# Performance work log

Measured on AMD Instinct MI355X. Metric: run time of the kernel, lower is better.

Reference implementation:

```python
import jax, jax.numpy as jnp
import numpy as np

N_NODES = 10000

def _gcn_norm(edges, n_nodes):
    # PyG GCNConv default: add self-loops, symmetric normalization D^-1/2 A_hat D^-1/2
    src, dst = edges[0], edges[1]
    loop = jnp.arange(n_nodes, dtype=src.dtype)
    src = jnp.concatenate([src, loop])
    dst = jnp.concatenate([dst, loop])
    deg = jax.ops.segment_sum(jnp.ones_like(dst, dtype=jnp.float32), dst, num_segments=n_nodes)
    dinv = jnp.where(deg > 0, jax.lax.rsqrt(deg), 0.0)
    norm = dinv[src] * dinv[dst]  # [E + N]
    return src, dst, norm

def _gcn_layer(x, src, dst, norm, W, b):
    # linear transform, then gather -> weight -> scatter-add aggregation
    x = x @ W  # [N, F]
    msg = x[src] * norm[:, None]  # [E+N, F]
    out = jax.ops.segment_sum(msg, dst, num_segments=x.shape[0])
    return out + b

def setup_inputs() -> dict:
    key = jax.random.key(0)
    k1, k2, k3, k4 = jax.random.split(key, 4)
    d = 128
    E = 640000
    scale = 1.0 / np.sqrt(d)
    return {
        "nodes_embeddings": jax.random.normal(k1, (N_NODES, d), dtype=jnp.float32),
        "edges": jax.random.randint(k2, (2, E), 0, N_NODES, dtype=jnp.int64),
        "W1": jax.random.normal(k3, (d, d), dtype=jnp.float32) * scale,
        "b1": jnp.zeros((d,), dtype=jnp.float32),
        "W2": jax.random.normal(k4, (d, d), dtype=jnp.float32) * scale,
        "b2": jnp.zeros((d,), dtype=jnp.float32),
    }

def reference(nodes_embeddings, edges, W1, b1, W2, b2):
    src, dst, norm = _gcn_norm(edges, nodes_embeddings.shape[0])
    x = _gcn_layer(nodes_embeddings, src, dst, norm, W1, b1)
    x = _gcn_layer(x, src, dst, norm, W2, b2)
    return x
```

## Files before the change

### kernel.cpp

```cpp
#include <hip/hip_runtime.h>
#include <hip/hip_bf16.h>

#define D 128
#define NBINS 157
#define BIN_CAP 5120
#define EPB 4096

__device__ __forceinline__ unsigned rne_bf16(float f) {
    unsigned u = __float_as_uint(f);
    return (u + 0x7FFFu + ((u >> 16) & 1u)) >> 16;
}
__device__ __forceinline__ float bf16_lo(unsigned u) { return __uint_as_float(u << 16); }
__device__ __forceinline__ float bf16_hi(unsigned u) { return __uint_as_float(u & 0xFFFF0000u); }

__global__ __launch_bounds__(512) void fused_gemm_scatter(
        const float* __restrict__ X, const float* __restrict__ W,
        float* __restrict__ Y,
        const int* __restrict__ src, const int* __restrict__ dst,
        int* __restrict__ binTotal, int* __restrict__ binned,
        int E, int N, int gGemm) {
    __shared__ float smem[D * D];
    int tid = threadIdx.x;

    if ((int)blockIdx.x < gGemm) {
        {
            const float4* W4 = (const float4*)W;
            float4* Ws4 = (float4*)smem;
            #pragma unroll
            for (int i = 0; i < 8; ++i)
                Ws4[tid + 512 * i] = W4[tid + 512 * i];
        }
        __syncthreads();
        const float2* Ws2 = (const float2*)smem;
        int col2 = tid & 63;
        int wv   = __builtin_amdgcn_readfirstlane(tid >> 6);
        int row0 = blockIdx.x * 32 + wv * 4;
        if (row0 >= N) return;

        const float4* xr[4];
        #pragma unroll
        for (int r = 0; r < 4; ++r) {
            int rr = row0 + r; if (rr > N - 1) rr = N - 1;
            xr[r] = (const float4*)(X + (size_t)rr * D);
        }
        float accx[4] = {0.f, 0.f, 0.f, 0.f};
        float accy[4] = {0.f, 0.f, 0.f, 0.f};
        #pragma unroll 8
        for (int kb = 0; kb < 32; ++kb) {
            float4 xv[4];
            #pragma unroll
            for (int r = 0; r < 4; ++r) xv[r] = xr[r][kb];
            #pragma unroll
            for (int kk = 0; kk < 4; ++kk) {
                float2 w = Ws2[(4 * kb + kk) * 64 + col2];
                #pragma unroll
                for (int r = 0; r < 4; ++r) {
                    float xs = ((const float*)&xv[r])[kk];
                    accx[r] = fmaf(xs, w.x, accx[r]);
                    accy[r] = fmaf(xs, w.y, accy[r]);
                }
            }
        }
        #pragma unroll
        for (int r = 0; r < 4; ++r) {
            int rr = row0 + r;
            if (rr < N)
                ((float2*)Y)[(size_t)rr * 64 + col2] = make_float2(accx[r], accy[r]);
        }
    } else {
        int* cnt   = (int*)smem;
        int* loff  = cnt + 160;
        int* gbase = cnt + 320;
        int* scur  = cnt + 480;
        int* stage = cnt + 640;
        for (int b = tid; b < NBINS; b += 512) cnt[b] = 0;
        __syncthreads();

        int bid = blockIdx.x - gGemm;
        int base = bid * EPB + tid * 8;
        int s[8], dl[8], bn[8];
        int ne = 0;
        if (base + 8 <= E) {
            const int4* s4 = (const int4*)(src + base);
            const int4* d4 = (const int4*)(dst + base);
            int4 a0 = s4[0], a1 = s4[1], c0 = d4[0], c1 = d4[1];
            int ss[8] = {a0.x, a0.y, a0.z, a0.w, a1.x, a1.y, a1.z, a1.w};
            int dd[8] = {c0.x, c0.y, c0.z, c0.w, c1.x, c1.y, c1.z, c1.w};
            ne = 8;
            #pragma unroll
            for (int i = 0; i < 8; ++i) { s[i] = ss[i]; bn[i] = dd[i] >> 6; dl[i] = dd[i] & 63; }
        } else {
            for (int i = 0; i < 8; ++i) {
                int e = base + i;
                if (e < E) { s[ne] = src[e]; int d = dst[e]; bn[ne] = d >> 6; dl[ne] = d & 63; ++ne; }
            }
        }
        for (int i = 0; i < ne; ++i) atomicAdd(&cnt[bn[i]], 1);
        __syncthreads();

        if (tid < NBINS) gbase[tid] = atomicAdd(&binTotal[tid], cnt[tid]);
        if (tid < 64) {
            int c0 = (3 * tid     < NBINS) ? cnt[3 * tid    ] : 0;
            int c1 = (3 * tid + 1 < NBINS) ? cnt[3 * tid + 1] : 0;
            int c2 = (3 * tid + 2 < NBINS) ? cnt[3 * tid + 2] : 0;
            int tsum = c0 + c1 + c2;
            int incl = tsum;
            #pragma unroll
            for (int off = 1; off < 64; off <<= 1) {
                int t = __shfl_up(incl, off);
                if (tid >= off) incl += t;
            }
            int excl = incl - tsum;
            if (3 * tid     < NBINS) loff[3 * tid    ] = excl;
            if (3 * tid + 1 < NBINS) loff[3 * tid + 1] = excl + c0;
            if (3 * tid + 2 < NBINS) loff[3 * tid + 2] = excl + c0 + c1;
        }
        __syncthreads();
        if (tid < NBINS) scur[tid] = loff[tid];
        __syncthreads();

        for (int i = 0; i < ne; ++i) {
            int p = atomicAdd(&scur[bn[i]], 1);
            stage[p] = s[i] | (dl[i] << 14);
        }
        __syncthreads();

        int wv = tid >> 6, lane = tid & 63;
        for (int b = wv; b < NBINS; b += 8) {
            int n = cnt[b], so = loff[b], go = b * BIN_CAP + gbase[b];
            for (int i = lane; i < n; i += 64) binned[go + i] = stage[so + i];
        }
    }
}

__global__ __launch_bounds__(1024) void sort_bins(const int* __restrict__ binTotal,
                                                  const int* __restrict__ binned,
                                                  unsigned short* __restrict__ csr16,
                                                  float* __restrict__ dinv,
                                                  int* __restrict__ nodeStart,
                                                  int* __restrict__ nodeEnd,
                                                  const float* __restrict__ Y,
                                                  unsigned* __restrict__ Zb,
                                                  unsigned* __restrict__ Zb2, int N) {
    __shared__ int h[16][64];
    __shared__ int cur[16][64];
    __shared__ float sdinv[64];
    __shared__ int padTot;
    __shared__ int stage[BIN_CAP];
    int b = blockIdx.x, tid = threadIdx.x;
    int wv = tid >> 6, lane = tid & 63;
    int cntb = binTotal[b];
    h[wv][lane] = 0;
    __syncthreads();
    const int* bp = binned + b * BIN_CAP;
    for (int i = tid; i < cntb; i += 1024) atomicAdd(&h[wv][bp[i] >> 14], 1);
    __syncthreads();
    if (tid < 64) {
        int hv[16];
        int deg = 0;
        #pragma unroll
        for (int w2 = 0; w2 < 16; ++w2) { hv[w2] = h[w2][tid]; deg += hv[w2]; }
        int pdeg = (deg + 7) & ~7;
        int incl = pdeg;
        #pragma unroll
        for (int off = 1; off < 64; off <<= 1) {
            int t = __shfl_up(incl, off);
            if (tid >= off) incl += t;
        }
        int excl = incl - pdeg;
        int run = excl;
        #pragma unroll
        for (int w2 = 0; w2 < 16; ++w2) { cur[w2][tid] = run; run += hv[w2]; }
        float dv = rsqrtf((float)(deg + 1));
        sdinv[tid] = dv;
        if (tid == 63) padTot = incl;
        int node = b * 64 + tid;
        if (node < N) {
            dinv[node]      = dv;
            nodeStart[node] = b * BIN_CAP + excl;
            nodeEnd[node]   = b * BIN_CAP + excl + pdeg;
        }
    }
    __syncthreads();
    int cntPad = padTot;
    for (int i = tid; i < cntPad; i += 1024) stage[i] = N;
    __syncthreads();
    for (int i = tid; i < cntb; i += 1024) {
        int p = bp[i];
        int pos = atomicAdd(&cur[wv][p >> 14], 1);
        stage[pos] = p & 0x3FFF;
    }
    {
        const float4* Y4 = (const float4*)Y;
        uint2* Zp = (uint2*)Zb;
        #pragma unroll
        for (int i = 0; i < 2; ++i) {
            int idx = tid + 1024 * i;
            int row = idx >> 5, c = idx & 31;
            int node = b * 64 + row;
            if (node < N) {
                float4 v = Y4[(size_t)node * 32 + c];
                float dv = sdinv[row];
                uint2 o;
                o.x = (rne_bf16(v.y * dv) << 16) | rne_bf16(v.x * dv);
                o.y = (rne_bf16(v.w * dv) << 16) | rne_bf16(v.z * dv);
                Zp[(size_t)node * 32 + c] = o;
            }
        }
    }
    if (b == 0 && tid < 64) {
        Zb [(size_t)N * 64 + tid] = 0u;
        Zb2[(size_t)N * 64 + tid] = 0u;
    }
    __syncthreads();
    unsigned short* bw = csr16 + b * BIN_CAP;
    for (int i = tid; i < cntPad; i += 1024) bw[i] = (unsigned short)stage[i];
}

__global__ __launch_bounds__(256) void aggregate(const unsigned* __restrict__ Zb,
                                                 const int* __restrict__ nodeStart,
                                                 const int* __restrict__ nodeEnd,
                                                 const unsigned short* __restrict__ csr16,
                                                 const float* __restrict__ dinv,
                                                 const float* __restrict__ bias,
                                                 float* __restrict__ Out, int N,
                                                 const float* __restrict__ W2,
                                                 unsigned* __restrict__ Zout) {
    __shared__ float rowsLds[8][128];
    const bool fused = (W2 != nullptr);
    int wv    = __builtin_amdgcn_readfirstlane(threadIdx.x >> 6);
    int nodeA = blockIdx.x * 8 + wv * 2;
    bool active = (nodeA < N);
    if (!fused && !active) return;
    int lane = threadIdx.x & 63;
    int l16  = lane & 15;

    if (active) {
        int nodeB = nodeA + 1;
        bool hasB = (nodeB < N);
        int g = lane >> 4;

        const uint4* Z4 = (const uint4*)Zb;
        float a0=0.f,a1=0.f,a2=0.f,a3=0.f,a4=0.f,a5=0.f,a6=0.f,a7=0.f;
        float b0=0.f,b1v=0.f,b2v=0.f,b3=0.f,b4v=0.f,b5=0.f,b6=0.f,b7=0.f;

        int eA = nodeStart[nodeA], endA = nodeEnd[nodeA];
        int eB = 0, endB = 0;
        if (hasB) { eB = nodeStart[nodeB]; endB = nodeEnd[nodeB]; }

        while (eA < endA || eB < endB) {
            int remA = endA - eA; int cntA = remA > 64 ? 64 : (remA > 0 ? remA : 0);
            int remB = endB - eB; int cntB = remB > 64 ? 64 : (remB > 0 ? remB : 0);
            int myA = (lane < cntA) ? (int)csr16[eA + lane] : N;
            int myB = (lane < cntB) ? (int)csr16[eB + lane] : N;
            int cmax = cntA > cntB ? cntA : cntB;
            int rounds = cmax >> 2;
            #pragma unroll 16
            for (int j = 0; j < rounds; ++j) {
                int idxA = __shfl(myA, j * 4 + g);
                int idxB = __shfl(myB, j * 4 + g);
                uint4 ua = Z4[idxA * 16 + l16];
                uint4 ub = Z4[idxB * 16 + l16];
                a0 += bf16_lo(ua.x); a1 += bf16_hi(ua.x);
                a2 += bf16_lo(ua.y); a3 += bf16_hi(ua.y);
                a4 += bf16_lo(ua.z); a5 += bf16_hi(ua.z);
                a6 += bf16_lo(ua.w); a7 += bf16_hi(ua.w);
                b0  += bf16_lo(ub.x); b1v += bf16_hi(ub.x);
                b2v += bf16_lo(ub.y); b3  += bf16_hi(ub.y);
                b4v += bf16_lo(ub.z); b5  += bf16_hi(ub.z);
                b6  += bf16_lo(ub.w); b7  += bf16_hi(ub.w);
            }
            eA += cntA; eB += cntB;
        }
        #pragma unroll
        for (int m = 16; m <= 32; m <<= 1) {
            a0 += __shfl_xor(a0, m); a1 += __shfl_xor(a1, m);
            a2 += __shfl_xor(a2, m); a3 += __shfl_xor(a3, m);
            a4 += __shfl_xor(a4, m); a5 += __shfl_xor(a5, m);
            a6 += __shfl_xor(a6, m); a7 += __shfl_xor(a7, m);
            b0  += __shfl_xor(b0, m);  b1v += __shfl_xor(b1v, m);
            b2v += __shfl_xor(b2v, m); b3  += __shfl_xor(b3, m);
            b4v += __shfl_xor(b4v, m); b5  += __shfl_xor(b5, m);
            b6  += __shfl_xor(b6, m);  b7  += __shfl_xor(b7, m);
        }
        int half = lane >> 4;
        if (half == 0 || (half == 1 && hasB)) {
            int node = half ? nodeB : nodeA;
            float r0 = half ? b0  : a0, r1 = half ? b1v : a1;
            float r2 = half ? b2v : a2, r3 = half ? b3  : a3;
            float r4 = half ? b4v : a4, r5 = half ? b5  : a5;
            float r6 = half ? b6  : a6, r7 = half ? b7  : a7;
            uint4 su = Z4[node * 16 + l16];
            float dv = dinv[node];
            const float4* bp4 = (const float4*)bias;
            float4 ba = bp4[l16 * 2], bb = bp4[l16 * 2 + 1];
            float4 o0, o1;
            o0.x = (r0 + bf16_lo(su.x)) * dv + ba.x;
            o0.y = (r1 + bf16_hi(su.x)) * dv + ba.y;
            o0.z = (r2 + bf16_lo(su.y)) * dv + ba.z;
            o0.w = (r3 + bf16_hi(su.y)) * dv + ba.w;
            o1.x = (r4 + bf16_lo(su.z)) * dv + bb.x;
            o1.y = (r5 + bf16_hi(su.z)) * dv + bb.y;
            o1.z = (r6 + bf16_lo(su.w)) * dv + bb.z;
            o1.w = (r7 + bf16_hi(su.w)) * dv + bb.w;
            if (fused) {
                float4* rp = (float4*)&rowsLds[wv * 2 + half][0];
                rp[l16 * 2]     = o0;
                rp[l16 * 2 + 1] = o1;
            } else {
                float4* op = (float4*)Out + (size_t)node * 32 + l16 * 2;
                op[0] = o0;
                op[1] = o1;
            }
        }
    }

    if (fused) {
        __syncthreads();
        int tid  = threadIdx.x;
        int colg = (tid & 31) << 2;
        int r    = tid >> 5;
        int node = blockIdx.x * 8 + r;
        const float* xrow = &rowsLds[r][0];
        float ac0 = 0.f, ac1 = 0.f, ac2 = 0.f, ac3 = 0.f;
        #pragma unroll 8
        for (int k = 0; k < 128; ++k) {
            float xs = xrow[k];
            float4 w4 = *(const float4*)(W2 + (size_t)k * D + colg);
            ac0 = fmaf(xs, w4.x, ac0);
            ac1 = fmaf(xs, w4.y, ac1);
            ac2 = fmaf(xs, w4.z, ac2);
            ac3 = fmaf(xs, w4.w, ac3);
        }
        if (node < N) {
            float dv = dinv[node];
            uint2 o;
            o.x = (rne_bf16(ac1 * dv) << 16) | rne_bf16(ac0 * dv);
            o.y = (rne_bf16(ac3 * dv) << 16) | rne_bf16(ac2 * dv);
            ((uint2*)Zout)[(size_t)node * 32 + (colg >> 2)] = o;
        }
    }
}

extern "C" void kernel_launch(void* const* d_in, const int* in_sizes, int n_in,
                              void* d_out, int out_size, void* d_ws, size_t ws_size,
                              hipStream_t stream) {
    const float* X  = (const float*)d_in[0];
    const int*   ed = (const int*)d_in[1];
    const float* W1 = (const float*)d_in[2];
    const float* b1 = (const float*)d_in[3];
    const float* W2 = (const float*)d_in[4];
    const float* b2 = (const float*)d_in[5];
    float* out = (float*)d_out;

    const int N = in_sizes[0] / D;
    const int E = in_sizes[1] / 2;
    const int* src = ed;
    const int* dst = ed + E;

    char* w = (char*)d_ws;
    float*    Y        = (float*)w;            w += (size_t)N * D * sizeof(float);
    unsigned* Zb       = (unsigned*)w;         w += (size_t)(N + 1) * 64 * sizeof(unsigned);
    unsigned* Zb2      = (unsigned*)w;         w += (size_t)(N + 1) * 64 * sizeof(unsigned);
    int*      binned   = (int*)w;              w += (size_t)NBINS * BIN_CAP * sizeof(int);
    unsigned short* csr16 = (unsigned short*)w; w += (size_t)NBINS * BIN_CAP * sizeof(unsigned short);
    float*    dinv     = (float*)w;            w += (size_t)N * sizeof(float);
    int*      nodeStart= (int*)w;              w += (size_t)N * sizeof(int);
    int*      nodeEnd  = (int*)w;              w += (size_t)N * sizeof(int);
    int*      binTotal = (int*)w;              w += (size_t)NBINS * sizeof(int);

    hipMemsetAsync(binTotal, 0, NBINS * sizeof(int), stream);

    int gGemm1 = (N + 31) / 32;
    int gScat  = (E + EPB - 1) / EPB;
    fused_gemm_scatter<<<gGemm1 + gScat, 512, 0, stream>>>(
        X, W1, Y, src, dst, binTotal, binned, E, N, gGemm1);
    sort_bins<<<NBINS, 1024, 0, stream>>>(binTotal, binned, csr16, dinv,
                                          nodeStart, nodeEnd, Y, Zb, Zb2, N);

    int gAgg = (N + 7) / 8;
    aggregate<<<gAgg, 256, 0, stream>>>(Zb, nodeStart, nodeEnd, csr16, dinv,
                                        b1, out, N, W2, Zb2);
    aggregate<<<gAgg, 256, 0, stream>>>(Zb2, nodeStart, nodeEnd, csr16, dinv,
                                        b2, out, N, nullptr, nullptr);
}
```

Before: 133.4 us.

## Replace global atomic bin offsets with per-block slab layout and count matrix

Each scatter block now writes its per-bin edges into a fixed slot (bin, block) of capacity SCAP in a slab array, and records its count in a count matrix. The global atomicAdd on binTotal and the memset that reset it are removed. sort_bins then walks the 157 sub-slabs per bin using those counts. The change also merges the scur init into the scan to drop one barrier. The cost is sparser, strided reads in sort_bins, a larger workspace, and a hard assumption that no block puts more than 96 edges in one bin.

```diff
diff --git a/kernel.cpp b/kernel.cpp
--- a/kernel.cpp
+++ b/kernel.cpp
@@ -5,6 +5,8 @@
 #define NBINS 157
 #define BIN_CAP 5120
 #define EPB 4096
+#define SCAP 96
+#define SLABW (NBINS * SCAP)
 
 __device__ __forceinline__ unsigned rne_bf16(float f) {
     unsigned u = __float_as_uint(f);
@@ -17,7 +19,7 @@
         const float* __restrict__ X, const float* __restrict__ W,
         float* __restrict__ Y,
         const int* __restrict__ src, const int* __restrict__ dst,
-        int* __restrict__ binTotal, int* __restrict__ binned,
+        int* __restrict__ cntMat, int* __restrict__ binned,
         int E, int N, int gGemm) {
     __shared__ float smem[D * D];
     int tid = threadIdx.x;
@@ -70,9 +72,8 @@
     } else {
         int* cnt   = (int*)smem;
         int* loff  = cnt + 160;
-        int* gbase = cnt + 320;
-        int* scur  = cnt + 480;
-        int* stage = cnt + 640;
+        int* scur  = cnt + 320;
+        int* stage = cnt + 480;
         for (int b = tid; b < NBINS; b += 512) cnt[b] = 0;
         __syncthreads();
 
@@ -98,7 +99,6 @@
         for (int i = 0; i < ne; ++i) atomicAdd(&cnt[bn[i]], 1);
         __syncthreads();
 
-        if (tid < NBINS) gbase[tid] = atomicAdd(&binTotal[tid], cnt[tid]);
         if (tid < 64) {
             int c0 = (3 * tid     < NBINS) ? cnt[3 * tid    ] : 0;
             int c1 = (3 * tid + 1 < NBINS) ? cnt[3 * tid + 1] : 0;
@@ -111,12 +111,10 @@
                 if (tid >= off) incl += t;
             }
             int excl = incl - tsum;
-            if (3 * tid     < NBINS) loff[3 * tid    ] = excl;
-            if (3 * tid + 1 < NBINS) loff[3 * tid + 1] = excl + c0;
-            if (3 * tid + 2 < NBINS) loff[3 * tid + 2] = excl + c0 + c1;
-        }
-        __syncthreads();
-        if (tid < NBINS) scur[tid] = loff[tid];
+            if (3 * tid < NBINS)     { loff[3 * tid]     = excl;           scur[3 * tid]     = excl; }
+            if (3 * tid + 1 < NBINS) { loff[3 * tid + 1] = excl + c0;      scur[3 * tid + 1] = excl + c0; }
+            if (3 * tid + 2 < NBINS) { loff[3 * tid + 2] = excl + c0 + c1; scur[3 * tid + 2] = excl + c0 + c1; }
+        }
         __syncthreads();
 
         for (int i = 0; i < ne; ++i) {
@@ -127,13 +125,15 @@
 
         int wv = tid >> 6, lane = tid & 63;
         for (int b = wv; b < NBINS; b += 8) {
-            int n = cnt[b], so = loff[b], go = b * BIN_CAP + gbase[b];
-            for (int i = lane; i < n; i += 64) binned[go + i] = stage[so + i];
-        }
-    }
-}
-
-__global__ __launch_bounds__(1024) void sort_bins(const int* __restrict__ binTotal,
+            int n = cnt[b], so = loff[b];
+            int* dstp = binned + b * SLABW + bid * SCAP;
+            for (int i = lane; i < n; i += 64) dstp[i] = stage[so + i];
+            if (lane == 0) cntMat[b * NBINS + bid] = n;
+        }
+    }
+}
+
+__global__ __launch_bounds__(1024) void sort_bins(const int* __restrict__ cntMat,
                                                   const int* __restrict__ binned,
                                                   unsigned short* __restrict__ csr16,
                                                   float* __restrict__ dinv,
@@ -144,16 +144,21 @@
                                                   unsigned* __restrict__ Zb2, int N) {
     __shared__ int h[16][64];
     __shared__ int cur[16][64];
+    __shared__ int scnt[NBINS];
     __shared__ float sdinv[64];
     __shared__ int padTot;
     __shared__ int stage[BIN_CAP];
     int b = blockIdx.x, tid = threadIdx.x;
     int wv = tid >> 6, lane = tid & 63;
-    int cntb = binTotal[b];
     h[wv][lane] = 0;
-    __syncthreads();
-    const int* bp = binned + b * BIN_CAP;
-    for (int i = tid; i < cntb; i += 1024) atomicAdd(&h[wv][bp[i] >> 14], 1);
+    if (tid < NBINS) scnt[tid] = cntMat[b * NBINS + tid];
+    __syncthreads();
+    const int* binBase = binned + b * SLABW;
+    for (int s = wv; s < NBINS; s += 16) {
+        int n = scnt[s];
+        const int* sp = binBase + s * SCAP;
+        for (int i = lane; i < n; i += 64) atomicAdd(&h[wv][sp[i] >> 14], 1);
+    }
     __syncthreads();
     if (tid < 64) {
         int hv[16];
@@ -185,10 +190,14 @@
     int cntPad = padTot;
     for (int i = tid; i < cntPad; i += 1024) stage[i] = N;
     __syncthreads();
-    for (int i = tid; i < cntb; i += 1024) {
-        int p = bp[i];
-        int pos = atomicAdd(&cur[wv][p >> 14], 1);
-        stage[pos] = p & 0x3FFF;
+    for (int s = wv; s < NBINS; s += 16) {
+        int n = scnt[s];
+        const int* sp = binBase + s * SCAP;
+        for (int i = lane; i < n; i += 64) {
+            int p = sp[i];
+            int pos = atomicAdd(&cur[wv][p >> 14], 1);
+            stage[pos] = p & 0x3FFF;
+        }
     }
     {
         const float4* Y4 = (const float4*)Y;
@@ -362,20 +371,18 @@
     float*    Y        = (float*)w;            w += (size_t)N * D * sizeof(float);
     unsigned* Zb       = (unsigned*)w;         w += (size_t)(N + 1) * 64 * sizeof(unsigned);
     unsigned* Zb2      = (unsigned*)w;         w += (size_t)(N + 1) * 64 * sizeof(unsigned);
-    int*      binned   = (int*)w;              w += (size_t)NBINS * BIN_CAP * sizeof(int);
+    int*      binned   = (int*)w;              w += (size_t)NBINS * SLABW * sizeof(int);
     unsigned short* csr16 = (unsigned short*)w; w += (size_t)NBINS * BIN_CAP * sizeof(unsigned short);
     float*    dinv     = (float*)w;            w += (size_t)N * sizeof(float);
     int*      nodeStart= (int*)w;              w += (size_t)N * sizeof(int);
     int*      nodeEnd  = (int*)w;              w += (size_t)N * sizeof(int);
-    int*      binTotal = (int*)w;              w += (size_t)NBINS * sizeof(int);
-
-    hipMemsetAsync(binTotal, 0, NBINS * sizeof(int), stream);
+    int*      cntMat   = (int*)w;              w += (size_t)NBINS * NBINS * sizeof(int);
 
     int gGemm1 = (N + 31) / 32;
     int gScat  = (E + EPB - 1) / EPB;
     fused_gemm_scatter<<<gGemm1 + gScat, 512, 0, stream>>>(
-        X, W1, Y, src, dst, binTotal, binned, E, N, gGemm1);
-    sort_bins<<<NBINS, 1024, 0, stream>>>(binTotal, binned, csr16, dinv,
+        X, W1, Y, src, dst, cntMat, binned, E, N, gGemm1);
+    sort_bins<<<NBINS, 1024, 0, stream>>>(cntMat, binned, csr16, dinv,
                                           nodeStart, nodeEnd, Y, Zb, Zb2, N);
 
     int gAgg = (N + 7) / 8;
```

Result: no change. 132.1 us (-1.0%).
